# Performance work log

Measured on AMD Instinct MI355X. Metric: run time of the kernel, lower is better.

Reference implementation:

```python
import jax, jax.numpy as jnp
import numpy as np

N_NODES = 50000
N_EDGES = 800000
IN_C, HID_C, OUT_C = 128, 64, 40
BN_EPS = 1e-5


def _gcn_conv(x, W, b, src, dst, n):
    # PyG GCNConv: linear transform, then symmetric-normalized sum aggregation
    h = x @ W  # [n, out_c]
    ones = jnp.ones(src.shape[0], dtype=h.dtype)
    deg = jax.ops.segment_sum(ones, dst, num_segments=n)  # in-degree incl. self-loops
    dinv = jnp.where(deg > 0, jax.lax.rsqrt(deg), 0.0)
    norm = dinv[src] * dinv[dst]  # [E]
    agg = jax.ops.segment_sum(h[src] * norm[:, None], dst, num_segments=n)
    return agg + b


def _bn_relu(x, gamma, beta, mean, var):
    # eval-mode BatchNorm1d fused with ReLU (dropout is identity in eval)
    return jax.nn.relu((x - mean) * jax.lax.rsqrt(var + BN_EPS) * gamma + beta)


def setup_inputs() -> dict:
    key = jax.random.key(0)
    ks = jax.random.split(key, 8)
    x = jax.random.normal(ks[0], (N_NODES, IN_C), dtype=jnp.float32)
    edge_index = jax.random.randint(ks[1], (2, N_EDGES), 0, N_NODES, dtype=jnp.int64)
    W0 = jax.random.normal(ks[2], (IN_C, HID_C), dtype=jnp.float32) / np.sqrt(IN_C)
    b0 = jnp.zeros((HID_C,), jnp.float32)
    W1 = jax.random.normal(ks[3], (HID_C, HID_C), dtype=jnp.float32) / np.sqrt(HID_C)
    b1 = jnp.zeros((HID_C,), jnp.float32)
    W2 = jax.random.normal(ks[4], (HID_C, OUT_C), dtype=jnp.float32) / np.sqrt(HID_C)
    b2 = jnp.zeros((OUT_C,), jnp.float32)
    gamma0 = jnp.ones((HID_C,), jnp.float32); beta0 = jnp.zeros((HID_C,), jnp.float32)
    mean0 = jnp.zeros((HID_C,), jnp.float32); var0 = jnp.ones((HID_C,), jnp.float32)
    gamma1 = jnp.ones((HID_C,), jnp.float32); beta1 = jnp.zeros((HID_C,), jnp.float32)
    mean1 = jnp.zeros((HID_C,), jnp.float32); var1 = jnp.ones((HID_C,), jnp.float32)
    return {
        "x": x, "edge_index": edge_index,
        "W0": W0, "b0": b0, "gamma0": gamma0, "beta0": beta0, "mean0": mean0, "var0": var0,
        "W1": W1, "b1": b1, "gamma1": gamma1, "beta1": beta1, "mean1": mean1, "var1": var1,
        "W2": W2, "b2": b2,
    }


def reference(x, edge_index, W0, b0, gamma0, beta0, mean0, var0,
              W1, b1, gamma1, beta1, mean1, var1, W2, b2):
    n = x.shape[0]
    loops = jnp.arange(n, dtype=edge_index.dtype)
    src = jnp.concatenate([edge_index[0], loops])
    dst = jnp.concatenate([edge_index[1], loops])

    h = _gcn_conv(x, W0, b0, src, dst, n)
    h = _bn_relu(h, gamma0, beta0, mean0, var0)
    h = _gcn_conv(h, W1, b1, src, dst, n)
    h = _bn_relu(h, gamma1, beta1, mean1, var1)
    out = _gcn_conv(h, W2, b2, src, dst, n)
    return out
```

## Files before the change

kernel.cpp:

```cpp
#include <hip/hip_runtime.h>
#include <hip/hip_fp16.h>

#define N_NODES 50000
#define N_EDGES 800000
#define BN_EPS 1e-5f

#define NBUCK 196
#define PART_CAP 6016
#define PB 196
#define GB 782

template <int WIDTH>
__device__ __forceinline__ int lds_scan_excl(int* s, int t, int v) {
    s[t] = v;
    __syncthreads();
    for (int off = 1; off < WIDTH; off <<= 1) {
        int x = (t >= off) ? s[t - off] : 0;
        __syncthreads();
        s[t] += x;
        __syncthreads();
    }
    return s[t] - v;
}

__device__ __forceinline__ unsigned src_phase(unsigned s) {
    return (s * 42950u) >> 29;
}

template <int K, int M, bool FOLD>
__device__ __forceinline__ void gemm_body(int bid, const float* __restrict__ X,
                                          const float* __restrict__ W,
                                          const float* __restrict__ gamma,
                                          const float* __restrict__ var,
                                          float* __restrict__ Hs, int n, float* lds) {
    constexpr int KC = 32;
    float* Xs = lds;
    float* Ws = lds + 64 * 36;
    float* bns = lds + 64 * 36 + 32 * M;
    int tid = threadIdx.x;
    int tx = tid & 15, ty = tid >> 4;
    int row0 = bid * 64;
    if (FOLD && tid < M) bns[tid] = gamma[tid] * rsqrtf(var[tid] + BN_EPS);
    __syncthreads();
    float acc[4][4] = {};
    for (int k0 = 0; k0 < K; k0 += KC) {
#pragma unroll
        for (int it = 0; it < 2; ++it) {
            int fi = tid + it * 256;
            int r = fi >> 3, q = fi & 7;
            int row = row0 + r;
            float4 v = make_float4(0.f, 0.f, 0.f, 0.f);
            if (row < n) v = *(const float4*)&X[(size_t)row * K + k0 + q * 4];
            *(float4*)&Xs[r * 36 + q * 4] = v;
        }
#pragma unroll
        for (int it = 0; it < 2; ++it) {
            int fi = tid + it * 256;
            int kk = fi >> 4, cw = (fi & 15) * 4;
            float4 w = *(const float4*)&W[(size_t)(k0 + kk) * M + cw];
            if (FOLD) { w.x *= bns[cw]; w.y *= bns[cw + 1]; w.z *= bns[cw + 2]; w.w *= bns[cw + 3]; }
            *(float4*)&Ws[kk * M + cw] = w;
        }
        __syncthreads();
#pragma unroll 8
        for (int kk = 0; kk < KC; ++kk) {
            float4 bv = *(float4*)&Ws[kk * M + tx * 4];
#pragma unroll
            for (int j = 0; j < 4; ++j) {
                float a = Xs[(ty * 4 + j) * 36 + kk];
                acc[j][0] += a * bv.x;
                acc[j][1] += a * bv.y;
                acc[j][2] += a * bv.z;
                acc[j][3] += a * bv.w;
            }
        }
        __syncthreads();
    }
#pragma unroll
    for (int j = 0; j < 4; ++j) {
        int r = row0 + ty * 4 + j;
        if (r < n) {
            float4 v = make_float4(acc[j][0], acc[j][1], acc[j][2], acc[j][3]);
            *(float4*)&Hs[(size_t)r * M + tx * 4] = v;
        }
    }
}

__global__ __launch_bounds__(256, 4)
void fused_gemm0_partition_kernel(const float* __restrict__ X, const float* __restrict__ W,
                                  const float* __restrict__ gamma, const float* __restrict__ var,
                                  float* __restrict__ Hs, int n,
                                  const int* __restrict__ src, const int* __restrict__ dst,
                                  int* __restrict__ gcur, unsigned int* __restrict__ part,
                                  int nE) {
    __shared__ float lds[64 * 36 + 32 * 64 + 64];
    if (blockIdx.x >= PB) {
        gemm_body<128, 64, true>(blockIdx.x - PB, X, W, gamma, var, Hs, n, lds);
        return;
    }
    int* lcnt  = (int*)lds;
    int* gbase = ((int*)lds) + 256;
    int t = threadIdx.x;
    int base = blockIdx.x * 4096;
    for (int i = t; i < NBUCK; i += 256) lcnt[i] = 0;
    __syncthreads();
    unsigned int val[16], pk[16];
#pragma unroll
    for (int i = 0; i < 16; ++i) {
        int e = base + i * 256 + t;
        if (e < nE) {
            unsigned s = (unsigned)src[e], d = (unsigned)dst[e];
            unsigned b = d >> 8;
            int r = atomicAdd(&lcnt[b], 1);
            val[i] = s | ((d & 255u) << 16);
            pk[i] = b | ((unsigned)r << 8);
        } else pk[i] = 0xffffffffu;
    }
    __syncthreads();
    for (int i = t; i < NBUCK; i += 256) gbase[i] = atomicAdd(&gcur[i], lcnt[i]);
    __syncthreads();
#pragma unroll
    for (int i = 0; i < 16; ++i) {
        if (pk[i] != 0xffffffffu) {
            unsigned b = pk[i] & 255u;
            unsigned p = (unsigned)gbase[b] + (pk[i] >> 8);
            if (p < PART_CAP) part[b * PART_CAP + p] = val[i];
        }
    }
}

__global__ __launch_bounds__(1024, 1)
void build_kernel(const unsigned int* __restrict__ part, const int* __restrict__ gcur,
                  int* __restrict__ rowptr, float* __restrict__ dinv,
                  unsigned short* __restrict__ csr, const float* __restrict__ Hs,
                  __half* __restrict__ Hh, int n) {
    __shared__ int buf[1024];
    __shared__ int nc4[1024], cur4[1024];
    __shared__ float sdinv[256];
    __shared__ unsigned short csr_lds[PART_CAP];
    __shared__ int sh[2];
    int b = blockIdx.x, t = threadIdx.x;

    int v = (t < NBUCK) ? gcur[t] : 0;
    int ex = lds_scan_excl<1024>(buf, t, v);
    if (t == b) { sh[0] = ex; sh[1] = v; }
    nc4[t] = 0;
    __syncthreads();
    int off = sh[0];
    int ec = sh[1] < PART_CAP ? sh[1] : PART_CAP;
    const unsigned int* pb = part + (size_t)b * PART_CAP;

    for (int i = t; i < ec; i += 1024) {
        unsigned w = pb[i];
        atomicAdd(&nc4[((w >> 16) & 255u) * 4 + src_phase(w & 0xffffu)], 1);
    }
    __syncthreads();

    int c = 0, c0 = 0, c1 = 0, c2 = 0;
    if (t < 256) {
        c0 = nc4[t * 4 + 0]; c1 = nc4[t * 4 + 1]; c2 = nc4[t * 4 + 2];
        c = c0 + c1 + c2 + nc4[t * 4 + 3];
    }
    int nx = lds_scan_excl<1024>(buf, t, c);
    if (t < 256) {
        cur4[t * 4 + 0] = nx;
        cur4[t * 4 + 1] = nx + c0;
        cur4[t * 4 + 2] = nx + c0 + c1;
        cur4[t * 4 + 3] = nx + c0 + c1 + c2;
        float dv = rsqrtf((float)c + 1.0f);
        sdinv[t] = dv;
        int node = b * 256 + t;
        if (node < n) {
            rowptr[node] = off + nx;
            dinv[node] = dv;
        }
    }
    if (b == NBUCK - 1 && t == 0) rowptr[n] = off + ec;
    __syncthreads();

    for (int i = t; i < ec; i += 1024) {
        unsigned w = pb[i];
        unsigned nd = (w >> 16) & 255u;
        unsigned s = w & 0xffffu;
        int p = atomicAdd(&cur4[nd * 4 + src_phase(s)], 1);
        csr_lds[p] = (unsigned short)s;
    }
    __syncthreads();
    for (int i = t; i < ec; i += 1024) csr[off + i] = csr_lds[i];

    const float4* H4 = (const float4*)(Hs + (size_t)b * 256 * 64);
    for (int i = t; i < 4096; i += 1024) {
        int nd = i >> 4;
        int nn = b * 256 + nd;
        if (nn < n) {
            float s = sdinv[nd];
            float4 x = H4[i];
            union { uint2 u; __half2 h[2]; } U;
            U.h[0] = __floats2half2_rn(x.x * s, x.y * s);
            U.h[1] = __floats2half2_rn(x.z * s, x.w * s);
            *(uint2*)&Hh[(size_t)nn * 64 + (i & 15) * 4] = U.u;
        }
    }
}

template <int MOUT, bool FOLD_NEXT>
__global__ __launch_bounds__(256, 5)
void gather_gemm_h(const __half* __restrict__ Hh, const int* __restrict__ rowptr,
                   const unsigned short* __restrict__ csr, const float* __restrict__ dinv,
                   const float* __restrict__ bb, const float* __restrict__ gamma,
                   const float* __restrict__ beta, const float* __restrict__ mean,
                   const float* __restrict__ var,
                   const float* __restrict__ Wn, const float* __restrict__ gn,
                   const float* __restrict__ vn, __half* __restrict__ Hout, int n) {
    __shared__ float zs[32 * 68];
    __shared__ float Ws[64 * MOUT];
    int t = threadIdx.x;
    int nd = t >> 3, l = t & 7;
    int d = blockIdx.x * 32 + nd;
    int c8 = l * 8;
    for (int i = t; i < 64 * MOUT; i += 256) {
        float w = Wn[i];
        if (FOLD_NEXT) { int c = i % MOUT; w *= gn[c] * rsqrtf(vn[c] + BN_EPS); }
        Ws[i] = w;
    }
    __syncthreads();
    float acc[8] = {};
    float di = 0.f;
    int beg = 0, end = 0;
    if (d < n) {
        beg = rowptr[d]; end = rowptr[d + 1];
        di = dinv[d];
        union { uint4 u; __half2 h[4]; } S;
        S.u = *(const uint4*)&Hh[(size_t)d * 64 + c8];
#pragma unroll
        for (int p = 0; p < 4; ++p) {
            float2 f = __half22float2(S.h[p]);
            acc[2 * p] += f.x; acc[2 * p + 1] += f.y;
        }
    }
    int e = beg;
    int head = (beg + 7) & ~7;
    if (head > end) head = end;
    for (; e < head; ++e) {
        int s = csr[e];
        union { uint4 u; __half2 h[4]; } V;
        V.u = *(const uint4*)&Hh[(size_t)s * 64 + c8];
#pragma unroll
        for (int p = 0; p < 4; ++p) {
            float2 f = __half22float2(V.h[p]);
            acc[2 * p] += f.x; acc[2 * p + 1] += f.y;
        }
    }
    for (; e + 8 <= end; e += 8) {
        uint4 iv = *(const uint4*)&csr[e];
        int sidx[8];
        sidx[0] = iv.x & 0xffff; sidx[1] = iv.x >> 16;
        sidx[2] = iv.y & 0xffff; sidx[3] = iv.y >> 16;
        sidx[4] = iv.z & 0xffff; sidx[5] = iv.z >> 16;
        sidx[6] = iv.w & 0xffff; sidx[7] = iv.w >> 16;
        uint4 vv[8];
#pragma unroll
        for (int q = 0; q < 8; ++q)
            vv[q] = *(const uint4*)&Hh[(size_t)sidx[q] * 64 + c8];
#pragma unroll
        for (int q = 0; q < 8; ++q) {
            union { uint4 u; __half2 h[4]; } V; V.u = vv[q];
#pragma unroll
            for (int p = 0; p < 4; ++p) {
                float2 f = __half22float2(V.h[p]);
                acc[2 * p] += f.x; acc[2 * p + 1] += f.y;
            }
        }
    }
    for (; e < end; ++e) {
        int s = csr[e];
        union { uint4 u; __half2 h[4]; } V;
        V.u = *(const uint4*)&Hh[(size_t)s * 64 + c8];
#pragma unroll
        for (int p = 0; p < 4; ++p) {
            float2 f = __half22float2(V.h[p]);
            acc[2 * p] += f.x; acc[2 * p + 1] += f.y;
        }
    }
    if (d < n) {
#pragma unroll
        for (int q = 0; q < 8; ++q) {
            int cc = c8 + q;
            float s0 = gamma[cc] * rsqrtf(var[cc] + BN_EPS);
            float bias = (bb[cc] - mean[cc]) * s0 + beta[cc];
            zs[nd * 68 + cc] = fmaxf(acc[q] * di + bias, 0.0f);
        }
    }
    asm volatile("s_waitcnt lgkmcnt(0)" ::: "memory");
    __builtin_amdgcn_sched_barrier(0);
    if (c8 < MOUT && d < n) {
        float o[8] = {};
        for (int k0 = 0; k0 < 64; k0 += 4) {
            float4 zq = *(const float4*)&zs[nd * 68 + k0];
#pragma unroll
            for (int j = 0; j < 4; ++j) {
                float zk = (&zq.x)[j];
                float4 w0 = *(const float4*)&Ws[(k0 + j) * MOUT + c8];
                float4 w1 = *(const float4*)&Ws[(k0 + j) * MOUT + c8 + 4];
                o[0] += zk * w0.x; o[1] += zk * w0.y; o[2] += zk * w0.z; o[3] += zk * w0.w;
                o[4] += zk * w1.x; o[5] += zk * w1.y; o[6] += zk * w1.z; o[7] += zk * w1.w;
            }
        }
        union { uint4 u; __half2 h[4]; } O;
#pragma unroll
        for (int p = 0; p < 4; ++p)
            O.h[p] = __floats2half2_rn(o[2 * p] * di, o[2 * p + 1] * di);
        *(uint4*)&Hout[(size_t)d * MOUT + c8] = O.u;
    }
}

__global__ __launch_bounds__(256, 6)
void gather_out_kernel(const __half* __restrict__ t3, const int* __restrict__ rowptr,
                       const unsigned short* __restrict__ csr, const float* __restrict__ dinv,
                       const float* __restrict__ bias, float* __restrict__ out, int n) {
    int t = threadIdx.x;
    if (t >= 250) return;
    int nd = t / 5, l = t % 5;
    int d = blockIdx.x * 50 + nd;
    if (d >= n) return;
    int c8 = l * 8;
    int beg = rowptr[d], end = rowptr[d + 1];
    float di = dinv[d];
    float acc[8];
    {
        union { uint4 u; __half2 h[4]; } S;
        S.u = *(const uint4*)&t3[(size_t)d * 40 + c8];
#pragma unroll
        for (int p = 0; p < 4; ++p) {
            float2 f = __half22float2(S.h[p]);
            acc[2 * p] = f.x; acc[2 * p + 1] = f.y;
        }
    }
    int e = beg;
    int head = (beg + 7) & ~7;
    if (head > end) head = end;
    for (; e < head; ++e) {
        int s = csr[e];
        union { uint4 u; __half2 h[4]; } V;
        V.u = *(const uint4*)&t3[(size_t)s * 40 + c8];
#pragma unroll
        for (int p = 0; p < 4; ++p) {
            float2 f = __half22float2(V.h[p]);
            acc[2 * p] += f.x; acc[2 * p + 1] += f.y;
        }
    }
    for (; e + 8 <= end; e += 8) {
        uint4 iv = *(const uint4*)&csr[e];
        int sidx[8];
        sidx[0] = iv.x & 0xffff; sidx[1] = iv.x >> 16;
        sidx[2] = iv.y & 0xffff; sidx[3] = iv.y >> 16;
        sidx[4] = iv.z & 0xffff; sidx[5] = iv.z >> 16;
        sidx[6] = iv.w & 0xffff; sidx[7] = iv.w >> 16;
        uint4 vv[8];
#pragma unroll
        for (int q = 0; q < 8; ++q)
            vv[q] = *(const uint4*)&t3[(size_t)sidx[q] * 40 + c8];
#pragma unroll
        for (int q = 0; q < 8; ++q) {
            union { uint4 u; __half2 h[4]; } V; V.u = vv[q];
#pragma unroll
            for (int p = 0; p < 4; ++p) {
                float2 f = __half22float2(V.h[p]);
                acc[2 * p] += f.x; acc[2 * p + 1] += f.y;
            }
        }
    }
    for (; e < end; ++e) {
        int s = csr[e];
        union { uint4 u; __half2 h[4]; } V;
        V.u = *(const uint4*)&t3[(size_t)s * 40 + c8];
#pragma unroll
        for (int p = 0; p < 4; ++p) {
            float2 f = __half22float2(V.h[p]);
            acc[2 * p] += f.x; acc[2 * p + 1] += f.y;
        }
    }
    float4 r0, r1;
    r0.x = acc[0] * di + bias[c8 + 0];
    r0.y = acc[1] * di + bias[c8 + 1];
    r0.z = acc[2] * di + bias[c8 + 2];
    r0.w = acc[3] * di + bias[c8 + 3];
    r1.x = acc[4] * di + bias[c8 + 4];
    r1.y = acc[5] * di + bias[c8 + 5];
    r1.z = acc[6] * di + bias[c8 + 6];
    r1.w = acc[7] * di + bias[c8 + 7];
    *(float4*)&out[(size_t)d * 40 + c8] = r0;
    *(float4*)&out[(size_t)d * 40 + c8 + 4] = r1;
}

extern "C" void kernel_launch(void* const* d_in, const int* in_sizes, int n_in,
                              void* d_out, int out_size, void* d_ws, size_t ws_size,
                              hipStream_t stream) {
    const float* x      = (const float*)d_in[0];
    const int*   ei     = (const int*)d_in[1];
    const float* W0     = (const float*)d_in[2];
    const float* b0     = (const float*)d_in[3];
    const float* gamma0 = (const float*)d_in[4];
    const float* beta0  = (const float*)d_in[5];
    const float* mean0  = (const float*)d_in[6];
    const float* var0   = (const float*)d_in[7];
    const float* W1     = (const float*)d_in[8];
    const float* b1     = (const float*)d_in[9];
    const float* gamma1 = (const float*)d_in[10];
    const float* beta1  = (const float*)d_in[11];
    const float* mean1  = (const float*)d_in[12];
    const float* var1   = (const float*)d_in[13];
    const float* W2     = (const float*)d_in[14];
    const float* b2     = (const float*)d_in[15];
    float* out = (float*)d_out;

    const int* srcp = ei;
    const int* dstp = ei + N_EDGES;
    const int N = N_NODES, E = N_EDGES;

    char* ws = (char*)d_ws;
    int*            gcur   = (int*)(ws + 0);
    int*            rowptr = (int*)(ws + 1024);
    float*          dinv   = (float*)(ws + 202240);
    unsigned short* csr    = (unsigned short*)(ws + 402688);
    float*          Hs     = (float*)(ws + 2002944);
    __half*         bufh   = (__half*)(ws + 2002944);
    __half*         t3h    = (__half*)(ws + 8402944);
    unsigned int*   part   = (unsigned int*)(ws + 14802944);
    __half*         Hh     = (__half*)(ws + 21202944);

    hipMemsetAsync(gcur, 0, NBUCK * sizeof(int), stream);

    fused_gemm0_partition_kernel<<<PB + GB, 256, 0, stream>>>(
        x, W0, gamma0, var0, Hs, N, srcp, dstp, gcur, part, E);

    build_kernel<<<NBUCK, 1024, 0, stream>>>(part, gcur, rowptr, dinv, csr, Hs, Hh, N);

    gather_gemm_h<64, true><<<(N + 31) / 32, 256, 0, stream>>>(
        Hh, rowptr, csr, dinv, b0, gamma0, beta0, mean0, var0,
        W1, gamma1, var1, bufh, N);

    gather_gemm_h<40, false><<<(N + 31) / 32, 256, 0, stream>>>(
        bufh, rowptr, csr, dinv, b1, gamma1, beta1, mean1, var1,
        W2, nullptr, nullptr, t3h, N);

    gather_out_kernel<<<N / 50, 256, 0, stream>>>(t3h, rowptr, csr, dinv, b2, out, N);
}
```

Before: 209.6 us.

## Pad each CSR row to a multiple of eight with a zero-row sentinel

The build kernel now pads every node's neighbor list to a multiple of 8 entries, filling the extra slots with a sentinel index that points at a zeroed feature row. Row pointers become (begin, end) pairs. This lets the gather kernels drop their scalar head and tail loops and run only the aligned 8-wide vectorized loop. In exchange it does extra gathers of the zero row (up to 7 per node), uses more CSR storage and LDS, and changes the workspace layout.

```diff
diff --git a/kernel.cpp b/kernel.cpp
--- a/kernel.cpp
+++ b/kernel.cpp
@@ -7,6 +7,9 @@
 
 #define NBUCK 196
 #define PART_CAP 6016
+#define BUCK_STRIDE 1800
+#define CSR_LDS_CAP 7808
+#define PAD_IDX 50000
 #define PB 196
 #define GB 782
 
@@ -131,22 +134,24 @@
 
 __global__ __launch_bounds__(1024, 1)
 void build_kernel(const unsigned int* __restrict__ part, const int* __restrict__ gcur,
-                  int* __restrict__ rowptr, float* __restrict__ dinv,
+                  uint2* __restrict__ rowptr, float* __restrict__ dinv,
                   unsigned short* __restrict__ csr, const float* __restrict__ Hs,
                   __half* __restrict__ Hh, int n) {
     __shared__ int buf[1024];
     __shared__ int nc4[1024], cur4[1024];
     __shared__ float sdinv[256];
-    __shared__ unsigned short csr_lds[PART_CAP];
+    __shared__ unsigned short csr_lds[CSR_LDS_CAP];
     __shared__ int sh[2];
     int b = blockIdx.x, t = threadIdx.x;
 
+    if (b == 0 && t < 8) ((uint4*)(Hh + (size_t)PAD_IDX * 64))[t] = make_uint4(0, 0, 0, 0);
+
     int v = (t < NBUCK) ? gcur[t] : 0;
     int ex = lds_scan_excl<1024>(buf, t, v);
-    if (t == b) { sh[0] = ex; sh[1] = v; }
+    if (t == b) { sh[0] = ((ex + 7) & ~7) + b * BUCK_STRIDE; sh[1] = v; }
     nc4[t] = 0;
     __syncthreads();
-    int off = sh[0];
+    int base = sh[0];
     int ec = sh[1] < PART_CAP ? sh[1] : PART_CAP;
     const unsigned int* pb = part + (size_t)b * PART_CAP;
 
@@ -156,12 +161,14 @@
     }
     __syncthreads();
 
-    int c = 0, c0 = 0, c1 = 0, c2 = 0;
+    int c = 0, c0 = 0, c1 = 0, c2 = 0, cp = 0;
     if (t < 256) {
         c0 = nc4[t * 4 + 0]; c1 = nc4[t * 4 + 1]; c2 = nc4[t * 4 + 2];
         c = c0 + c1 + c2 + nc4[t * 4 + 3];
-    }
-    int nx = lds_scan_excl<1024>(buf, t, c);
+        cp = (c + 7) & ~7;
+    }
+    int nx = lds_scan_excl<1024>(buf, t, cp);
+    int ptot = buf[1023];
     if (t < 256) {
         cur4[t * 4 + 0] = nx;
         cur4[t * 4 + 1] = nx + c0;
@@ -171,11 +178,10 @@
         sdinv[t] = dv;
         int node = b * 256 + t;
         if (node < n) {
-            rowptr[node] = off + nx;
+            rowptr[node] = make_uint2((unsigned)(base + nx), (unsigned)(base + nx + cp));
             dinv[node] = dv;
         }
     }
-    if (b == NBUCK - 1 && t == 0) rowptr[n] = off + ec;
     __syncthreads();
 
     for (int i = t; i < ec; i += 1024) {
@@ -185,8 +191,11 @@
         int p = atomicAdd(&cur4[nd * 4 + src_phase(s)], 1);
         csr_lds[p] = (unsigned short)s;
     }
-    __syncthreads();
-    for (int i = t; i < ec; i += 1024) csr[off + i] = csr_lds[i];
+    if (t < 256) {
+        for (int i = nx + c; i < nx + cp; ++i) csr_lds[i] = (unsigned short)PAD_IDX;
+    }
+    __syncthreads();
+    for (int i = t; i < ptot; i += 1024) csr[base + i] = csr_lds[i];
 
     const float4* H4 = (const float4*)(Hs + (size_t)b * 256 * 64);
     for (int i = t; i < 4096; i += 1024) {
@@ -205,7 +214,7 @@
 
 template <int MOUT, bool FOLD_NEXT>
 __global__ __launch_bounds__(256, 5)
-void gather_gemm_h(const __half* __restrict__ Hh, const int* __restrict__ rowptr,
+void gather_gemm_h(const __half* __restrict__ Hh, const uint2* __restrict__ rowptr,
                    const unsigned short* __restrict__ csr, const float* __restrict__ dinv,
                    const float* __restrict__ bb, const float* __restrict__ gamma,
                    const float* __restrict__ beta, const float* __restrict__ mean,
@@ -218,6 +227,7 @@
     int nd = t >> 3, l = t & 7;
     int d = blockIdx.x * 32 + nd;
     int c8 = l * 8;
+    if (blockIdx.x == 0 && t < MOUT) Hout[(size_t)PAD_IDX * MOUT + t] = __float2half(0.f);
     for (int i = t; i < 64 * MOUT; i += 256) {
         float w = Wn[i];
         if (FOLD_NEXT) { int c = i % MOUT; w *= gn[c] * rsqrtf(vn[c] + BN_EPS); }
@@ -226,9 +236,10 @@
     __syncthreads();
     float acc[8] = {};
     float di = 0.f;
-    int beg = 0, end = 0;
+    int e = 0, end = 0;
     if (d < n) {
-        beg = rowptr[d]; end = rowptr[d + 1];
+        uint2 rp = rowptr[d];
+        e = (int)rp.x; end = (int)rp.y;
         di = dinv[d];
         union { uint4 u; __half2 h[4]; } S;
         S.u = *(const uint4*)&Hh[(size_t)d * 64 + c8];
@@ -238,20 +249,7 @@
             acc[2 * p] += f.x; acc[2 * p + 1] += f.y;
         }
     }
-    int e = beg;
-    int head = (beg + 7) & ~7;
-    if (head > end) head = end;
-    for (; e < head; ++e) {
-        int s = csr[e];
-        union { uint4 u; __half2 h[4]; } V;
-        V.u = *(const uint4*)&Hh[(size_t)s * 64 + c8];
-#pragma unroll
-        for (int p = 0; p < 4; ++p) {
-            float2 f = __half22float2(V.h[p]);
-            acc[2 * p] += f.x; acc[2 * p + 1] += f.y;
-        }
-    }
-    for (; e + 8 <= end; e += 8) {
+    for (; e < end; e += 8) {
         uint4 iv = *(const uint4*)&csr[e];
         int sidx[8];
         sidx[0] = iv.x & 0xffff; sidx[1] = iv.x >> 16;
@@ -272,16 +270,6 @@
             }
         }
     }
-    for (; e < end; ++e) {
-        int s = csr[e];
-        union { uint4 u; __half2 h[4]; } V;
-        V.u = *(const uint4*)&Hh[(size_t)s * 64 + c8];
-#pragma unroll
-        for (int p = 0; p < 4; ++p) {
-            float2 f = __half22float2(V.h[p]);
-            acc[2 * p] += f.x; acc[2 * p + 1] += f.y;
-        }
-    }
     if (d < n) {
 #pragma unroll
         for (int q = 0; q < 8; ++q) {
@@ -315,7 +303,7 @@
 }
 
 __global__ __launch_bounds__(256, 6)
-void gather_out_kernel(const __half* __restrict__ t3, const int* __restrict__ rowptr,
+void gather_out_kernel(const __half* __restrict__ t3, const uint2* __restrict__ rowptr,
                        const unsigned short* __restrict__ csr, const float* __restrict__ dinv,
                        const float* __restrict__ bias, float* __restrict__ out, int n) {
     int t = threadIdx.x;
@@ -324,7 +312,8 @@
     int d = blockIdx.x * 50 + nd;
     if (d >= n) return;
     int c8 = l * 8;
-    int beg = rowptr[d], end = rowptr[d + 1];
+    uint2 rp = rowptr[d];
+    int e = (int)rp.x, end = (int)rp.y;
     float di = dinv[d];
     float acc[8];
     {
@@ -336,20 +325,7 @@
             acc[2 * p] = f.x; acc[2 * p + 1] = f.y;
         }
     }
-    int e = beg;
-    int head = (beg + 7) & ~7;
-    if (head > end) head = end;
-    for (; e < head; ++e) {
-        int s = csr[e];
-        union { uint4 u; __half2 h[4]; } V;
-        V.u = *(const uint4*)&t3[(size_t)s * 40 + c8];
-#pragma unroll
-        for (int p = 0; p < 4; ++p) {
-            float2 f = __half22float2(V.h[p]);
-            acc[2 * p] += f.x; acc[2 * p + 1] += f.y;
-        }
-    }
-    for (; e + 8 <= end; e += 8) {
+    for (; e < end; e += 8) {
         uint4 iv = *(const uint4*)&csr[e];
         int sidx[8];
         sidx[0] = iv.x & 0xffff; sidx[1] = iv.x >> 16;
@@ -368,16 +344,6 @@
                 float2 f = __half22float2(V.h[p]);
                 acc[2 * p] += f.x; acc[2 * p + 1] += f.y;
             }
-        }
-    }
-    for (; e < end; ++e) {
-        int s = csr[e];
-        union { uint4 u; __half2 h[4]; } V;
-        V.u = *(const uint4*)&t3[(size_t)s * 40 + c8];
-#pragma unroll
-        for (int p = 0; p < 4; ++p) {
-            float2 f = __half22float2(V.h[p]);
-            acc[2 * p] += f.x; acc[2 * p + 1] += f.y;
         }
     }
     float4 r0, r1;
@@ -420,14 +386,14 @@
 
     char* ws = (char*)d_ws;
     int*            gcur   = (int*)(ws + 0);
-    int*            rowptr = (int*)(ws + 1024);
-    float*          dinv   = (float*)(ws + 202240);
-    unsigned short* csr    = (unsigned short*)(ws + 402688);
-    float*          Hs     = (float*)(ws + 2002944);
-    __half*         bufh   = (__half*)(ws + 2002944);
-    __half*         t3h    = (__half*)(ws + 8402944);
-    unsigned int*   part   = (unsigned int*)(ws + 14802944);
-    __half*         Hh     = (__half*)(ws + 21202944);
+    uint2*          rowptr = (uint2*)(ws + 1024);
+    float*          dinv   = (float*)(ws + 401152);
+    unsigned short* csr    = (unsigned short*)(ws + 601344);
+    float*          Hs     = (float*)(ws + 2960896);
+    __half*         bufh   = (__half*)(ws + 2960896);
+    __half*         t3h    = (__half*)(ws + 9361152);
+    unsigned int*   part   = (unsigned int*)(ws + 15761152);
+    __half*         Hh     = (__half*)(ws + 20477952);
 
     hipMemsetAsync(gcur, 0, NBUCK * sizeof(int), stream);
 
```

New measurement: 184.6 us. -11.9%, faster.
